# Kernel tuning notes

Hardware: AMD Instinct MI355X
Metric: run time of the kernel (lower is better)

## Reference

```python
import jax, jax.numpy as jnp
import numpy as np

N = 50000
IN_DIM, HID_DIM, OUT_DIM = 16, 64, 32


def setup_inputs() -> dict:
    key = jax.random.key(0)
    k1, k2, k3, k4, k5 = jax.random.split(key, 5)
    x = jax.random.normal(k1, (N, IN_DIM), dtype=jnp.float32)
    edge_index = jax.random.randint(k2, (2, 800000), 0, N, dtype=jnp.int64)
    # GCNConv weights (glorot-ish scale) and biases
    W1 = jax.random.normal(k3, (IN_DIM, HID_DIM), dtype=jnp.float32) / np.sqrt(IN_DIM)
    b1 = jnp.zeros((HID_DIM,), dtype=jnp.float32)
    W2 = jax.random.normal(k4, (HID_DIM, OUT_DIM), dtype=jnp.float32) / np.sqrt(HID_DIM)
    b2 = jnpplus = jnp.zeros((OUT_DIM,), dtype=jnp.float32)
    return {"x": x, "edge_index": edge_index, "W1": W1, "b1": b1, "W2": W2, "b2": b2}


def _gcn_conv(x, src, dst, norm, W, b, num_nodes):
    # PyG GCNConv: h = X W; out[d] = sum_e norm_e * h[src_e]; out += b
    h = x @ W                                   # [N, D_out] small GEMM
    msgs = h[src] * norm[:, None]               # [E+N, D_out] gather (memory-bound)
    out = jax.ops.segment_sum(msgs, dst, num_segments=num_nodes)  # scatter-add
    return out + b


def reference(x, edge_index, W1, b1, W2, b2):
    num_nodes = x.shape[0]
    # add self-loops (PyG GCNConv default add_self_loops=True)
    loops = jnp.arange(num_nodes, dtype=edge_index.dtype)
    src = jnp.concatenate([edge_index[0], loops])
    dst = jnp.concatenate([edge_index[1], loops])
    # symmetric normalization D^{-1/2} (A+I) D^{-1/2}, degree over dst
    deg = jax.ops.segment_sum(jnp.ones_like(src, dtype=x.dtype), dst, num_segments=num_nodes)
    dinv = jnp.where(deg > 0, jax.lax.rsqrt(deg), 0.0)
    norm = dinv[src] * dinv[dst]                # [E+N]

    h = _gcn_conv(x, src, dst, norm, W1, b1, num_nodes)
    h = jax.nn.relu(h)
    out = _gcn_conv(h, src, dst, norm, W2, b2, num_nodes)
    return out
```

## Files before the change

### kernel.cpp

```cpp
#include <hip/hip_runtime.h>
#include <hip/hip_fp16.h>

#define IN_DIM  16
#define HID_DIM 64
#define OUT_DIM 32

#define CAP 8192
#define EPB 3328

__device__ __forceinline__ int detect_is64(const void* edges) {
    const int* w = (const int*)edges;
    int is64 = 1;
    #pragma unroll
    for (int i = 0; i < 16; ++i) is64 &= (w[2 * i + 1] == 0);
    return is64;
}

__device__ __forceinline__ long long edge_at(const void* edges, int is64, long long i) {
    if (is64) return ((const long long*)edges)[i];
    return (long long)((const int*)edges)[i];
}

__global__ __launch_bounds__(256) void k_partA(const void* edges, int* gcur,
                                               unsigned int* gpart, int nbuk, long long E) {
    __shared__ unsigned int staged[EPB];
    __shared__ int hcnt[256], hoff[256], hcur[256];
    __shared__ int s64s;
    int t = threadIdx.x;
    if (t == 0) s64s = detect_is64(edges);
    hcnt[t] = 0;
    __syncthreads();
    int is64 = s64s;

    long long e0 = (long long)blockIdx.x * EPB;
    unsigned int rs[13], rd[13];
    int nval = 0;
    #pragma unroll
    for (int k = 0; k < 13; ++k) {
        long long e = e0 + t + k * 256;
        if (e < E) {
            rs[k] = (unsigned int)edge_at(edges, is64, e);
            rd[k] = (unsigned int)edge_at(edges, is64, E + e);
            atomicAdd(&hcnt[rd[k] >> 8], 1);
            nval = k + 1;
        }
    }
    __syncthreads();

    int v = hcnt[t];
    hoff[t] = v;
    __syncthreads();
    for (int d = 1; d < 256; d <<= 1) {
        int u = (t >= d) ? hoff[t - d] : 0;
        __syncthreads();
        hoff[t] += u;
        __syncthreads();
    }
    int excl = hoff[t] - v;
    hoff[t] = excl;
    hcur[t] = excl;
    __syncthreads();

    #pragma unroll
    for (int k = 0; k < 13; ++k) {
        if (k < nval) {
            int p = atomicAdd(&hcur[rd[k] >> 8], 1);
            staged[p] = rs[k] | ((rd[k] & 255u) << 16);
        }
    }
    __syncthreads();

    if (t < nbuk) {
        int c = hcnt[t];
        if (c > 0) {
            int base = atomicAdd(&gcur[t], c);
            int o = hoff[t];
            for (int k = 0; k < c; ++k) {
                int idx = base + k;
                if (idx < CAP) gpart[(size_t)t * CAP + idx] = staged[o + k];
            }
        }
    }
}

__global__ __launch_bounds__(256) void k_partB(const int* __restrict__ gcur,
                                               const unsigned int* __restrict__ gpart,
                                               unsigned short* __restrict__ csr,
                                               int* __restrict__ offs,
                                               float* __restrict__ dinv,
                                               int nbuk, int N) {
    __shared__ unsigned int ebuf[CAP];
    __shared__ int bscan[256];
    __shared__ int hcnt[256], hoff[256], hcur[256];
    int t = threadIdx.x;
    int b = blockIdx.x;

    int bc = (t < nbuk) ? min(gcur[t], CAP) : 0;
    bscan[t] = bc;
    hcnt[t] = 0;
    __syncthreads();
    for (int d = 1; d < 256; d <<= 1) {
        int u = (t >= d) ? bscan[t - d] : 0;
        __syncthreads();
        bscan[t] += u;
        __syncthreads();
    }
    int base = (b == 0) ? 0 : bscan[b - 1];
    int cnt  = bscan[b] - base;

    for (int i = t; i < cnt; i += 256) ebuf[i] = gpart[(size_t)b * CAP + i];
    __syncthreads();
    for (int i = t; i < cnt; i += 256) atomicAdd(&hcnt[(ebuf[i] >> 16) & 255u], 1);
    __syncthreads();

    int v = hcnt[t];
    hoff[t] = v;
    __syncthreads();
    for (int d = 1; d < 256; d <<= 1) {
        int u = (t >= d) ? hoff[t - d] : 0;
        __syncthreads();
        hoff[t] += u;
        __syncthreads();
    }
    int excl = hoff[t] - v;
    hcur[t] = excl;
    __syncthreads();

    int node = b * 256 + t;
    if (node < N) {
        offs[node] = base + excl;
        dinv[node] = rsqrtf((float)v + 1.0f);
    }
    if (b == nbuk - 1 && t == 0) offs[N] = bscan[nbuk - 1];

    for (int i = t; i < cnt; i += 256) {
        unsigned int e = ebuf[i];
        int dl = (e >> 16) & 255;
        int p = atomicAdd(&hcur[dl], 1);
        csr[base + p] = (unsigned short)(e & 0xffffu);
    }
}

__global__ __launch_bounds__(256) void k_agg1(
    const float* __restrict__ x, const float* __restrict__ dinv,
    const int* __restrict__ offs, const unsigned short* __restrict__ csr,
    float* __restrict__ aggX, int N)
{
    int node = (blockIdx.x * 256 + threadIdx.x) >> 6;
    if (node >= N) return;
    int lane = threadIdx.x & 63;
    int comp = lane & 3;
    int g    = lane >> 2;
    const float4* x4 = (const float4*)x;
    float di = dinv[node];
    int start = offs[node], end = offs[node + 1];
    float4 acc = make_float4(0.f, 0.f, 0.f, 0.f);
    if (g == 0) {
        float4 xs = x4[(size_t)node * 4 + comp];
        acc = make_float4(di * xs.x, di * xs.y, di * xs.z, di * xs.w);
    }
    for (int j = start + g; j < end; j += 16) {
        int s = csr[j];
        float w = dinv[s];
        float4 xv = x4[(size_t)s * 4 + comp];
        acc.x += w * xv.x; acc.y += w * xv.y;
        acc.z += w * xv.z; acc.w += w * xv.w;
    }
    #pragma unroll
    for (int m = 4; m < 64; m <<= 1) {
        acc.x += __shfl_xor(acc.x, m, 64);
        acc.y += __shfl_xor(acc.y, m, 64);
        acc.z += __shfl_xor(acc.z, m, 64);
        acc.w += __shfl_xor(acc.w, m, 64);
    }
    if (g == 0)
        ((float4*)aggX)[(size_t)node * 4 + comp] =
            make_float4(di * acc.x, di * acc.y, di * acc.z, di * acc.w);
}

#define AGG_P 20
#define H1_P  68
__global__ __launch_bounds__(256) void k_gemm12(
    const float* __restrict__ aggX,
    const float* __restrict__ W1, const float* __restrict__ b1,
    const float* __restrict__ W2, __half* __restrict__ h2, int N)
{
    __shared__ float W1s[IN_DIM * HID_DIM];
    __shared__ float W2s[HID_DIM * OUT_DIM];
    __shared__ float b1s[HID_DIM];
    __shared__ float aggs[64 * AGG_P];
    __shared__ float h1s[64 * H1_P];

    int tid = threadIdx.x;
    int base = blockIdx.x * 64;
    for (int i = tid; i < IN_DIM * HID_DIM; i += 256) W1s[i] = W1[i];
    for (int i = tid; i < HID_DIM * OUT_DIM; i += 256) W2s[i] = W2[i];
    if (tid < HID_DIM) b1s[tid] = b1[tid];

    {
        int node = tid >> 2, comp = tid & 3;
        float4 v = (base + node < N) ? ((const float4*)aggX)[(size_t)(base + node) * 4 + comp]
                                     : make_float4(0.f, 0.f, 0.f, 0.f);
        *(float4*)&aggs[node * AGG_P + comp * 4] = v;
    }
    __syncthreads();

    int node = tid >> 2, q = tid & 3;

    {
        float acc[16];
        #pragma unroll
        for (int c = 0; c < 16; ++c) acc[c] = b1s[q * 16 + c];
        #pragma unroll
        for (int k = 0; k < IN_DIM; ++k) {
            float a = aggs[node * AGG_P + k];
            const float4* wr = (const float4*)&W1s[k * HID_DIM + q * 16];
            #pragma unroll
            for (int c4 = 0; c4 < 4; ++c4) {
                float4 w = wr[c4];
                acc[c4 * 4 + 0] += a * w.x; acc[c4 * 4 + 1] += a * w.y;
                acc[c4 * 4 + 2] += a * w.z; acc[c4 * 4 + 3] += a * w.w;
            }
        }
        float4* h1row = (float4*)&h1s[node * H1_P + q * 16];
        #pragma unroll
        for (int c4 = 0; c4 < 4; ++c4)
            h1row[c4] = make_float4(fmaxf(acc[c4 * 4 + 0], 0.f), fmaxf(acc[c4 * 4 + 1], 0.f),
                                    fmaxf(acc[c4 * 4 + 2], 0.f), fmaxf(acc[c4 * 4 + 3], 0.f));
    }
    __syncthreads();

    {
        float acc2[8];
        #pragma unroll
        for (int c = 0; c < 8; ++c) acc2[c] = 0.f;
        const float4* h1row = (const float4*)&h1s[node * H1_P];
        #pragma unroll
        for (int k4 = 0; k4 < 16; ++k4) {
            float4 hv = h1row[k4];
            float hvv[4] = {hv.x, hv.y, hv.z, hv.w};
            #pragma unroll
            for (int kk = 0; kk < 4; ++kk) {
                int k = k4 * 4 + kk;
                const float4* wr = (const float4*)&W2s[k * OUT_DIM + q * 8];
                float4 w0 = wr[0], w1 = wr[1];
                acc2[0] += hvv[kk] * w0.x; acc2[1] += hvv[kk] * w0.y;
                acc2[2] += hvv[kk] * w0.z; acc2[3] += hvv[kk] * w0.w;
                acc2[4] += hvv[kk] * w1.x; acc2[5] += hvv[kk] * w1.y;
                acc2[6] += hvv[kk] * w1.z; acc2[7] += hvv[kk] * w1.w;
            }
        }
        if (base + node < N) {
            __half2 p[4];
            #pragma unroll
            for (int c = 0; c < 4; ++c)
                p[c] = __floats2half2_rn(acc2[c * 2], acc2[c * 2 + 1]);
            ((uint4*)h2)[(size_t)(base + node) * 4 + q] = *(uint4*)p;
        }
    }
}

__global__ __launch_bounds__(256) void k_agg2(
    const __half* __restrict__ h2, const float* __restrict__ dinv,
    const int* __restrict__ offs, const unsigned short* __restrict__ csr,
    const float* __restrict__ b2, float* __restrict__ out, int N)
{
    int node = (blockIdx.x * 256 + threadIdx.x) >> 6;
    if (node >= N) return;
    int lane = threadIdx.x & 63;
    int comp = lane & 3;
    int way  = lane >> 2;
    const uint4* h24 = (const uint4*)h2;
    float di = dinv[node];
    int start = offs[node], end = offs[node + 1];
    float acc[8] = {0.f, 0.f, 0.f, 0.f, 0.f, 0.f, 0.f, 0.f};
    if (way == 0) {
        uint4 r = h24[(size_t)node * 4 + comp];
        const __half2* hp = (const __half2*)&r;
        #pragma unroll
        for (int c = 0; c < 4; ++c) {
            float2 f = __half22float2(hp[c]);
            acc[c * 2]     = di * f.x;
            acc[c * 2 + 1] = di * f.y;
        }
    }
    for (int j = start + way; j < end; j += 16) {
        int s = csr[j];
        float w = dinv[s];
        uint4 r = h24[(size_t)s * 4 + comp];
        const __half2* hp = (const __half2*)&r;
        #pragma unroll
        for (int c = 0; c < 4; ++c) {
            float2 f = __half22float2(hp[c]);
            acc[c * 2]     += w * f.x;
            acc[c * 2 + 1] += w * f.y;
        }
    }
    #pragma unroll
    for (int m = 4; m < 64; m <<= 1) {
        #pragma unroll
        for (int c = 0; c < 8; ++c) acc[c] += __shfl_xor(acc[c], m, 64);
    }
    if (way == 0) {
        const float4* b24 = (const float4*)b2;
        float4 bb0 = b24[comp * 2], bb1 = b24[comp * 2 + 1];
        float4* out4 = (float4*)out;
        out4[(size_t)node * 8 + comp * 2 + 0] =
            make_float4(di * acc[0] + bb0.x, di * acc[1] + bb0.y,
                        di * acc[2] + bb0.z, di * acc[3] + bb0.w);
        out4[(size_t)node * 8 + comp * 2 + 1] =
            make_float4(di * acc[4] + bb1.x, di * acc[5] + bb1.y,
                        di * acc[6] + bb1.z, di * acc[7] + bb1.w);
    }
}

extern "C" void kernel_launch(void* const* d_in, const int* in_sizes, int n_in,
                              void* d_out, int out_size, void* d_ws, size_t ws_size,
                              hipStream_t stream) {
    const float* x     = (const float*)d_in[0];
    const void*  edges = d_in[1];
    const float* W1    = (const float*)d_in[2];
    const float* b1    = (const float*)d_in[3];
    const float* W2    = (const float*)d_in[4];
    const float* b2    = (const float*)d_in[5];
    float* out = (float*)d_out;

    const int       N = in_sizes[0] / IN_DIM;
    const long long E = in_sizes[1] / 2;
    const int    NBUK = (N + 255) >> 8;

    unsigned short* csr   = (unsigned short*)d_ws;
    unsigned int*   gpart = (unsigned int*)(csr + ((E + 7) & ~7LL));
    float*  aggX     = (float*)(gpart + (size_t)NBUK * CAP);
    __half* h2       = (__half*)(aggX + (size_t)IN_DIM * N);
    float*  dinv     = (float*)(h2 + (size_t)OUT_DIM * N);
    int*    offs     = (int*)(dinv + N);
    int*    gcur     = offs + N + 1;

    const int B = 256;
    hipMemsetAsync(gcur, 0, (size_t)NBUK * sizeof(int), stream);
    k_partA<<<(int)((E + EPB - 1) / EPB), B, 0, stream>>>(edges, gcur, gpart, NBUK, E);
    k_partB<<<NBUK, B, 0, stream>>>(gcur, gpart, csr, offs, dinv, NBUK, N);

    k_agg1<<<(N + 3) / 4, B, 0, stream>>>(x, dinv, offs, csr, aggX, N);
    k_gemm12<<<(N + 63) / 64, B, 0, stream>>>(aggX, W1, b1, W2, h2, N);
    k_agg2<<<(N + 3) / 4, B, 0, stream>>>(h2, dinv, offs, csr, b2, out, N);
}
```

Before: 148.6 us.

## Replace atomic bucket partition with per-block stripes; pack four nodes per wave in aggregation

Partitioning no longer uses global atomic bucket cursors and a memset. Each partition block writes fixed-size stripes plus a count table, which the bucket kernel scans to gather edges deterministically. The aggregation kernels now handle four nodes per wavefront with four edge-ways each, unrolled two edges per step, which cuts idle lanes for low-degree nodes and shortens the shuffle reduction. Stripe capacity of 64 edges per block-bucket can silently drop edges on skewed graphs, and the count reduction adds strided reads.

```diff
diff --git a/kernel.cpp b/kernel.cpp
--- a/kernel.cpp
+++ b/kernel.cpp
@@ -5,8 +5,9 @@
 #define HID_DIM 64
 #define OUT_DIM 32
 
-#define CAP 8192
-#define EPB 3328
+#define CAP    8192
+#define EPB    3328
+#define STRIPE 64
 
 __device__ __forceinline__ int detect_is64(const void* edges) {
     const int* w = (const int*)edges;
@@ -21,8 +22,10 @@
     return (long long)((const int*)edges)[i];
 }
 
-__global__ __launch_bounds__(256) void k_partA(const void* edges, int* gcur,
-                                               unsigned int* gpart, int nbuk, long long E) {
+__global__ __launch_bounds__(256) void k_partA(const void* edges,
+                                               int* __restrict__ gcnt,
+                                               unsigned int* __restrict__ gpart,
+                                               int nbuk, int nblkA, long long E) {
     __shared__ unsigned int staged[EPB];
     __shared__ int hcnt[256], hoff[256], hcur[256];
     __shared__ int s64s;
@@ -70,46 +73,65 @@
     }
     __syncthreads();
 
-    if (t < nbuk) {
-        int c = hcnt[t];
-        if (c > 0) {
-            int base = atomicAdd(&gcur[t], c);
-            int o = hoff[t];
-            for (int k = 0; k < c; ++k) {
-                int idx = base + k;
-                if (idx < CAP) gpart[(size_t)t * CAP + idx] = staged[o + k];
-            }
-        }
-    }
-}
-
-__global__ __launch_bounds__(256) void k_partB(const int* __restrict__ gcur,
+    int wid = t >> 6, lane = t & 63;
+    for (int b = wid; b < nbuk; b += 4) {
+        int c = min(hcnt[b], STRIPE);
+        int o = hoff[b];
+        unsigned int* dstp = gpart + ((size_t)b * nblkA + blockIdx.x) * STRIPE;
+        if (lane < c) dstp[lane] = staged[o + lane];
+        if (lane == 0) gcnt[(size_t)blockIdx.x * nbuk + b] = c;
+    }
+}
+
+__global__ __launch_bounds__(256) void k_partB(const int* __restrict__ gcnt,
                                                const unsigned int* __restrict__ gpart,
                                                unsigned short* __restrict__ csr,
                                                int* __restrict__ offs,
                                                float* __restrict__ dinv,
-                                               int nbuk, int N) {
+                                               int nbuk, int nblkA, int N) {
     __shared__ unsigned int ebuf[CAP];
-    __shared__ int bscan[256];
+    __shared__ int btot[256];
+    __shared__ int scnt[256], soff[256];
     __shared__ int hcnt[256], hoff[256], hcur[256];
     int t = threadIdx.x;
     int b = blockIdx.x;
 
-    int bc = (t < nbuk) ? min(gcur[t], CAP) : 0;
-    bscan[t] = bc;
+    int tot = 0;
+    if (t < nbuk)
+        for (int i = 0; i < nblkA; ++i) tot += gcnt[(size_t)i * nbuk + t];
+    btot[t] = tot;
     hcnt[t] = 0;
     __syncthreads();
     for (int d = 1; d < 256; d <<= 1) {
-        int u = (t >= d) ? bscan[t - d] : 0;
-        __syncthreads();
-        bscan[t] += u;
-        __syncthreads();
-    }
-    int base = (b == 0) ? 0 : bscan[b - 1];
-    int cnt  = bscan[b] - base;
-
-    for (int i = t; i < cnt; i += 256) ebuf[i] = gpart[(size_t)b * CAP + i];
-    __syncthreads();
+        int u = (t >= d) ? btot[t - d] : 0;
+        __syncthreads();
+        btot[t] += u;
+        __syncthreads();
+    }
+    int base = (b == 0) ? 0 : btot[b - 1];
+    int cnt  = btot[b] - base;
+
+    int sv = (t < nblkA) ? gcnt[(size_t)t * nbuk + b] : 0;
+    scnt[t] = sv;
+    soff[t] = sv;
+    __syncthreads();
+    for (int d = 1; d < 256; d <<= 1) {
+        int u = (t >= d) ? soff[t - d] : 0;
+        __syncthreads();
+        soff[t] += u;
+        __syncthreads();
+    }
+    soff[t] -= sv;
+    __syncthreads();
+
+    int wid = t >> 6, lane = t & 63;
+    for (int i = wid; i < nblkA; i += 4) {
+        int c = scnt[i];
+        const unsigned int* srcp = gpart + ((size_t)b * nblkA + i) * STRIPE;
+        if (lane < c) ebuf[soff[i] + lane] = srcp[lane];
+    }
+    __syncthreads();
+
     for (int i = t; i < cnt; i += 256) atomicAdd(&hcnt[(ebuf[i] >> 16) & 255u], 1);
     __syncthreads();
 
@@ -131,7 +153,7 @@
         offs[node] = base + excl;
         dinv[node] = rsqrtf((float)v + 1.0f);
     }
-    if (b == nbuk - 1 && t == 0) offs[N] = bscan[nbuk - 1];
+    if (b == nbuk - 1 && t == 0) offs[N] = btot[nbuk - 1];
 
     for (int i = t; i < cnt; i += 256) {
         unsigned int e = ebuf[i];
@@ -146,34 +168,43 @@
     const int* __restrict__ offs, const unsigned short* __restrict__ csr,
     float* __restrict__ aggX, int N)
 {
-    int node = (blockIdx.x * 256 + threadIdx.x) >> 6;
+    int gtid = blockIdx.x * 256 + threadIdx.x;
+    int lane = gtid & 63;
+    int g = lane >> 4, sub = lane & 15;
+    int comp = sub & 3, way = sub >> 2;
+    int node = (gtid >> 6) * 4 + g;
     if (node >= N) return;
-    int lane = threadIdx.x & 63;
-    int comp = lane & 3;
-    int g    = lane >> 2;
     const float4* x4 = (const float4*)x;
     float di = dinv[node];
     int start = offs[node], end = offs[node + 1];
     float4 acc = make_float4(0.f, 0.f, 0.f, 0.f);
-    if (g == 0) {
+    if (way == 0) {
         float4 xs = x4[(size_t)node * 4 + comp];
         acc = make_float4(di * xs.x, di * xs.y, di * xs.z, di * xs.w);
     }
-    for (int j = start + g; j < end; j += 16) {
+    int j = start + way;
+    for (; j + 4 < end; j += 8) {
+        int s0 = csr[j], s1 = csr[j + 4];
+        float w0 = dinv[s0], w1 = dinv[s1];
+        float4 a0 = x4[(size_t)s0 * 4 + comp];
+        float4 a1 = x4[(size_t)s1 * 4 + comp];
+        acc.x += w0 * a0.x + w1 * a1.x; acc.y += w0 * a0.y + w1 * a1.y;
+        acc.z += w0 * a0.z + w1 * a1.z; acc.w += w0 * a0.w + w1 * a1.w;
+    }
+    if (j < end) {
         int s = csr[j];
         float w = dinv[s];
-        float4 xv = x4[(size_t)s * 4 + comp];
-        acc.x += w * xv.x; acc.y += w * xv.y;
-        acc.z += w * xv.z; acc.w += w * xv.w;
-    }
-    #pragma unroll
-    for (int m = 4; m < 64; m <<= 1) {
+        float4 a = x4[(size_t)s * 4 + comp];
+        acc.x += w * a.x; acc.y += w * a.y; acc.z += w * a.z; acc.w += w * a.w;
+    }
+    #pragma unroll
+    for (int m = 4; m <= 8; m <<= 1) {
         acc.x += __shfl_xor(acc.x, m, 64);
         acc.y += __shfl_xor(acc.y, m, 64);
         acc.z += __shfl_xor(acc.z, m, 64);
         acc.w += __shfl_xor(acc.w, m, 64);
     }
-    if (g == 0)
+    if (way == 0)
         ((float4*)aggX)[(size_t)node * 4 + comp] =
             make_float4(di * acc.x, di * acc.y, di * acc.z, di * acc.w);
 }
@@ -265,11 +296,12 @@
     const int* __restrict__ offs, const unsigned short* __restrict__ csr,
     const float* __restrict__ b2, float* __restrict__ out, int N)
 {
-    int node = (blockIdx.x * 256 + threadIdx.x) >> 6;
+    int gtid = blockIdx.x * 256 + threadIdx.x;
+    int lane = gtid & 63;
+    int g = lane >> 4, sub = lane & 15;
+    int comp = sub & 3, way = sub >> 2;
+    int node = (gtid >> 6) * 4 + g;
     if (node >= N) return;
-    int lane = threadIdx.x & 63;
-    int comp = lane & 3;
-    int way  = lane >> 2;
     const uint4* h24 = (const uint4*)h2;
     float di = dinv[node];
     int start = offs[node], end = offs[node + 1];
@@ -284,7 +316,23 @@
             acc[c * 2 + 1] = di * f.y;
         }
     }
-    for (int j = start + way; j < end; j += 16) {
+    int j = start + way;
+    for (; j + 4 < end; j += 8) {
+        int s0 = csr[j], s1 = csr[j + 4];
+        float w0 = dinv[s0], w1 = dinv[s1];
+        uint4 r0 = h24[(size_t)s0 * 4 + comp];
+        uint4 r1 = h24[(size_t)s1 * 4 + comp];
+        const __half2* hp0 = (const __half2*)&r0;
+        const __half2* hp1 = (const __half2*)&r1;
+        #pragma unroll
+        for (int c = 0; c < 4; ++c) {
+            float2 f0 = __half22float2(hp0[c]);
+            float2 f1 = __half22float2(hp1[c]);
+            acc[c * 2]     += w0 * f0.x + w1 * f1.x;
+            acc[c * 2 + 1] += w0 * f0.y + w1 * f1.y;
+        }
+    }
+    if (j < end) {
         int s = csr[j];
         float w = dinv[s];
         uint4 r = h24[(size_t)s * 4 + comp];
@@ -297,7 +345,7 @@
         }
     }
     #pragma unroll
-    for (int m = 4; m < 64; m <<= 1) {
+    for (int m = 4; m <= 8; m <<= 1) {
         #pragma unroll
         for (int c = 0; c < 8; ++c) acc[c] += __shfl_xor(acc[c], m, 64);
     }
@@ -328,21 +376,21 @@
     const int       N = in_sizes[0] / IN_DIM;
     const long long E = in_sizes[1] / 2;
     const int    NBUK = (N + 255) >> 8;
+    const int   NBLKA = (int)((E + EPB - 1) / EPB);
 
     unsigned short* csr   = (unsigned short*)d_ws;
     unsigned int*   gpart = (unsigned int*)(csr + ((E + 7) & ~7LL));
-    float*  aggX     = (float*)(gpart + (size_t)NBUK * CAP);
+    int*    gcnt     = (int*)(gpart + (size_t)NBUK * NBLKA * STRIPE);
+    float*  aggX     = (float*)(gcnt + (size_t)NBLKA * NBUK);
     __half* h2       = (__half*)(aggX + (size_t)IN_DIM * N);
     float*  dinv     = (float*)(h2 + (size_t)OUT_DIM * N);
     int*    offs     = (int*)(dinv + N);
-    int*    gcur     = offs + N + 1;
 
     const int B = 256;
-    hipMemsetAsync(gcur, 0, (size_t)NBUK * sizeof(int), stream);
-    k_partA<<<(int)((E + EPB - 1) / EPB), B, 0, stream>>>(edges, gcur, gpart, NBUK, E);
-    k_partB<<<NBUK, B, 0, stream>>>(gcur, gpart, csr, offs, dinv, NBUK, N);
-
-    k_agg1<<<(N + 3) / 4, B, 0, stream>>>(x, dinv, offs, csr, aggX, N);
+    k_partA<<<NBLKA, B, 0, stream>>>(edges, gcnt, gpart, NBUK, NBLKA, E);
+    k_partB<<<NBUK, B, 0, stream>>>(gcnt, gpart, csr, offs, dinv, NBUK, NBLKA, N);
+
+    k_agg1<<<(N + 15) / 16, B, 0, stream>>>(x, dinv, offs, csr, aggX, N);
     k_gemm12<<<(N + 63) / 64, B, 0, stream>>>(aggX, W1, b1, W2, h2, N);
-    k_agg2<<<(N + 3) / 4, B, 0, stream>>>(h2, dinv, offs, csr, b2, out, N);
-}
+    k_agg2<<<(N + 15) / 16, B, 0, stream>>>(h2, dinv, offs, csr, b2, out, N);
+}
```

After: 203.5 us. 1.37x slower.

## Pack four nodes per wavefront in aggregation kernels and unroll edge loop by two

Applied to the files above, without the earlier changes.

Both aggregation kernels now give each node 16 lanes (4 edge ways by 4 components) instead of a full 64-lane wavefront, so one wave processes four nodes. The average degree is about 17, so most of the 16 ways were idle before; the shuffle reduction shrinks to two steps and the grid is cut fourfold. The edge loop is unrolled by two to keep two independent gathers in flight per lane. The cost is more serial iterations per lane for high-degree nodes and possible load imbalance between the four nodes sharing a wave.

```diff
diff --git a/kernel.cpp b/kernel.cpp
--- a/kernel.cpp
+++ b/kernel.cpp
@@ -146,34 +146,43 @@
     const int* __restrict__ offs, const unsigned short* __restrict__ csr,
     float* __restrict__ aggX, int N)
 {
-    int node = (blockIdx.x * 256 + threadIdx.x) >> 6;
+    int gtid = blockIdx.x * 256 + threadIdx.x;
+    int lane = gtid & 63;
+    int g = lane >> 4, sub = lane & 15;
+    int comp = sub & 3, way = sub >> 2;
+    int node = (gtid >> 6) * 4 + g;
     if (node >= N) return;
-    int lane = threadIdx.x & 63;
-    int comp = lane & 3;
-    int g    = lane >> 2;
     const float4* x4 = (const float4*)x;
     float di = dinv[node];
     int start = offs[node], end = offs[node + 1];
     float4 acc = make_float4(0.f, 0.f, 0.f, 0.f);
-    if (g == 0) {
+    if (way == 0) {
         float4 xs = x4[(size_t)node * 4 + comp];
         acc = make_float4(di * xs.x, di * xs.y, di * xs.z, di * xs.w);
     }
-    for (int j = start + g; j < end; j += 16) {
+    int j = start + way;
+    for (; j + 4 < end; j += 8) {
+        int s0 = csr[j], s1 = csr[j + 4];
+        float w0 = dinv[s0], w1 = dinv[s1];
+        float4 a0 = x4[(size_t)s0 * 4 + comp];
+        float4 a1 = x4[(size_t)s1 * 4 + comp];
+        acc.x += w0 * a0.x + w1 * a1.x; acc.y += w0 * a0.y + w1 * a1.y;
+        acc.z += w0 * a0.z + w1 * a1.z; acc.w += w0 * a0.w + w1 * a1.w;
+    }
+    if (j < end) {
         int s = csr[j];
         float w = dinv[s];
-        float4 xv = x4[(size_t)s * 4 + comp];
-        acc.x += w * xv.x; acc.y += w * xv.y;
-        acc.z += w * xv.z; acc.w += w * xv.w;
-    }
-    #pragma unroll
-    for (int m = 4; m < 64; m <<= 1) {
+        float4 a = x4[(size_t)s * 4 + comp];
+        acc.x += w * a.x; acc.y += w * a.y; acc.z += w * a.z; acc.w += w * a.w;
+    }
+    #pragma unroll
+    for (int m = 4; m <= 8; m <<= 1) {
         acc.x += __shfl_xor(acc.x, m, 64);
         acc.y += __shfl_xor(acc.y, m, 64);
         acc.z += __shfl_xor(acc.z, m, 64);
         acc.w += __shfl_xor(acc.w, m, 64);
     }
-    if (g == 0)
+    if (way == 0)
         ((float4*)aggX)[(size_t)node * 4 + comp] =
             make_float4(di * acc.x, di * acc.y, di * acc.z, di * acc.w);
 }
@@ -265,11 +274,12 @@
     const int* __restrict__ offs, const unsigned short* __restrict__ csr,
     const float* __restrict__ b2, float* __restrict__ out, int N)
 {
-    int node = (blockIdx.x * 256 + threadIdx.x) >> 6;
+    int gtid = blockIdx.x * 256 + threadIdx.x;
+    int lane = gtid & 63;
+    int g = lane >> 4, sub = lane & 15;
+    int comp = sub & 3, way = sub >> 2;
+    int node = (gtid >> 6) * 4 + g;
     if (node >= N) return;
-    int lane = threadIdx.x & 63;
-    int comp = lane & 3;
-    int way  = lane >> 2;
     const uint4* h24 = (const uint4*)h2;
     float di = dinv[node];
     int start = offs[node], end = offs[node + 1];
@@ -284,7 +294,23 @@
             acc[c * 2 + 1] = di * f.y;
         }
     }
-    for (int j = start + way; j < end; j += 16) {
+    int j = start + way;
+    for (; j + 4 < end; j += 8) {
+        int s0 = csr[j], s1 = csr[j + 4];
+        float w0 = dinv[s0], w1 = dinv[s1];
+        uint4 r0 = h24[(size_t)s0 * 4 + comp];
+        uint4 r1 = h24[(size_t)s1 * 4 + comp];
+        const __half2* hp0 = (const __half2*)&r0;
+        const __half2* hp1 = (const __half2*)&r1;
+        #pragma unroll
+        for (int c = 0; c < 4; ++c) {
+            float2 f0 = __half22float2(hp0[c]);
+            float2 f1 = __half22float2(hp1[c]);
+            acc[c * 2]     += w0 * f0.x + w1 * f1.x;
+            acc[c * 2 + 1] += w0 * f0.y + w1 * f1.y;
+        }
+    }
+    if (j < end) {
         int s = csr[j];
         float w = dinv[s];
         uint4 r = h24[(size_t)s * 4 + comp];
@@ -297,7 +323,7 @@
         }
     }
     #pragma unroll
-    for (int m = 4; m < 64; m <<= 1) {
+    for (int m = 4; m <= 8; m <<= 1) {
         #pragma unroll
         for (int c = 0; c < 8; ++c) acc[c] += __shfl_xor(acc[c], m, 64);
     }
@@ -342,7 +368,7 @@
     k_partA<<<(int)((E + EPB - 1) / EPB), B, 0, stream>>>(edges, gcur, gpart, NBUK, E);
     k_partB<<<NBUK, B, 0, stream>>>(gcur, gpart, csr, offs, dinv, NBUK, N);
 
-    k_agg1<<<(N + 3) / 4, B, 0, stream>>>(x, dinv, offs, csr, aggX, N);
+    k_agg1<<<(N + 15) / 16, B, 0, stream>>>(x, dinv, offs, csr, aggX, N);
     k_gemm12<<<(N + 63) / 64, B, 0, stream>>>(aggX, W1, b1, W2, h2, N);
-    k_agg2<<<(N + 3) / 4, B, 0, stream>>>(h2, dinv, offs, csr, b2, out, N);
-}
+    k_agg2<<<(N + 15) / 16, B, 0, stream>>>(h2, dinv, offs, csr, b2, out, N);
+}
```

Result: faster. 137.5 us (-7.5%).
